# Kernel optimization log

Measured on AMD Instinct MI355X. Metric: run time of the kernel, lower is better.

Reference implementation:

```python
import jax, jax.numpy as jnp
import numpy as np

RX = 1024
RY = 1024
F = 4
HID = 64
N = 2097152


def setup_inputs() -> dict:
    key = jax.random.key(0)
    ks = jax.random.split(key, 8)
    x = jax.random.uniform(ks[0], (N, 3), dtype=jnp.float32)  # (id, u, v) in [0,1)
    emb = jax.random.uniform(ks[1], (RX * RY, F), dtype=jnp.float32) * 2.0 - 1.0
    din = 1 + F  # id feature + interpolated grid feature
    w1 = jax.random.normal(ks[2], (din, HID), dtype=jnp.float32) / np.sqrt(din)
    b1 = jnp.zeros((HID,), dtype=jnp.float32)
    w2 = jax.random.normal(ks[3], (HID, HID), dtype=jnp.float32) / np.sqrt(HID)
    b2 = jnp.zeros((HID,), dtype=jnp.float32)
    w3 = jax.random.normal(ks[4], (HID, 3), dtype=jnp.float32) / np.sqrt(HID)
    b3 = jnp.zeros((3,), dtype=jnp.float32)
    return {"x": x, "emb": emb, "w1": w1, "b1": b1, "w2": w2, "b2": b2, "w3": w3, "b3": b3}


def _grid_features(uv, emb):
    u, v = uv[:, 0], uv[:, 1]
    # vertex ids of bounding cell, faithful to the torch edge handling
    x0 = (u * RX).astype(jnp.int32)
    x0 = jnp.where(x0 == RX, 0, x0)          # wrap exactly-1.0 to 0
    x1 = jnp.where(x0 + 1 == RX, RX - 1, x0 + 1)
    y0 = (v * RY).astype(jnp.int32)
    y1 = jnp.where(y0 + 1 == RY, RY - 1, y0 + 1)
    # weights computed AFTER the x0 wrap, as in the original
    wx = (u * RX - x0.astype(jnp.float32))[:, None]
    wy = (v * RY - y0.astype(jnp.float32))[:, None]
    # four gathers from the flat [RX*RY, F] table (row index = y*RX + x)
    v00 = emb[y0 * RX + x0]
    v10 = emb[y0 * RX + x1]
    v01 = emb[y1 * RX + x0]
    v11 = emb[y1 * RX + x1]
    vup = v00 * (1.0 - wx) + v10 * wx
    vdn = v01 * (1.0 - wx) + v11 * wx
    return vup * (1.0 - wy) + vdn * wy


def reference(x, emb, w1, b1, w2, b2, w3, b3):
    idf = x[:, :1]
    dgf = _grid_features(x[:, 1:3], emb)
    h = jnp.concatenate([idf, dgf], axis=1)   # [N, 5]
    h = jax.nn.relu(h @ w1 + b1)
    h = jax.nn.relu(h @ w2 + b2)
    return jax.nn.sigmoid(h @ w3 + b3)        # [N, 3]
```

## Files before the change

### kernel.cpp

```cpp
#include <hip/hip_runtime.h>
#include <hip/hip_bf16.h>


typedef __attribute__((ext_vector_type(8))) short bf16x8;
typedef __attribute__((ext_vector_type(4))) float f32x4;
typedef __attribute__((ext_vector_type(2))) unsigned int u32x2;
typedef __attribute__((ext_vector_type(4))) unsigned int u32x4;
typedef unsigned long long u64t;

#define HID 64

static __device__ __forceinline__ unsigned short f2bf(float f) {
    __hip_bfloat16 h = __float2bfloat16(f);
    return __builtin_bit_cast(unsigned short, h);
}
static __device__ __forceinline__ unsigned cvt_pk_bf16(float a, float b) {
    unsigned r;
    asm("v_cvt_pk_bf16_f32 %0, %1, %2" : "=v"(r) : "v"(a), "v"(b));
    return r;
}
static __device__ __forceinline__ void lds_fence() {
    asm volatile("s_waitcnt lgkmcnt(0)" ::: "memory");
}
#define MFMA16(a,b,c) __builtin_amdgcn_mfma_f32_16x16x32_bf16((a),(b),(c),0,0,0)

static __device__ __forceinline__ f32x4 unpk2(unsigned lo, unsigned hi) {
    f32x4 r;
    r[0] = __builtin_bit_cast(float, lo << 16);
    r[1] = __builtin_bit_cast(float, lo & 0xFFFF0000u);
    r[2] = __builtin_bit_cast(float, hi << 16);
    r[3] = __builtin_bit_cast(float, hi & 0xFFFF0000u);
    return r;
}
static __device__ __forceinline__ bf16x8 pack_pair(f32x4 lo, f32x4 hi) {
    u32x4 w;
    w[0] = cvt_pk_bf16(fmaxf(lo[0], 0.f), fmaxf(lo[1], 0.f));
    w[1] = cvt_pk_bf16(fmaxf(lo[2], 0.f), fmaxf(lo[3], 0.f));
    w[2] = cvt_pk_bf16(fmaxf(hi[0], 0.f), fmaxf(hi[1], 0.f));
    w[3] = cvt_pk_bf16(fmaxf(hi[2], 0.f), fmaxf(hi[3], 0.f));
    return __builtin_bit_cast(bf16x8, w);
}

struct TFrags {
    bf16x8 a1[4];
    bf16x8 a2[4][2];
    bf16x8 a3[2];
    f32x4  bias2[4];
    f32x4  bias3;
};

static __device__ __forceinline__ void build_tfrags(
    float* Wst, int tid, int cl, int kg,
    const float* __restrict__ w1, const float* __restrict__ b1,
    const float* __restrict__ w2, const float* __restrict__ b2,
    const float* __restrict__ w3, const float* __restrict__ b3, TFrags& F)
{
    {
        const f32x4* w2v = (const f32x4*)w2;
        f32x4* Wv = (f32x4*)Wst;
        #pragma unroll
        for (int i = 0; i < 4; ++i) Wv[tid + 256 * i] = w2v[tid + 256 * i];
        for (int idx = tid; idx < 320; idx += 256) Wst[4096 + idx] = w1[idx];
        if (tid < 64)  Wst[4416 + tid] = b1[tid];
        if (tid < 192) Wst[4480 + tid] = w3[tid];
        if (tid < 64)  Wst[4672 + tid] = b2[tid];
        if (tid < 3)   Wst[4736 + tid] = b3[tid];
    }
    __syncthreads();

    #pragma unroll
    for (int mt = 0; mt < 4; ++mt) {
        bf16x8 f = {};
        if (kg == 0) {
            int hid = mt * 16 + cl;
            #pragma unroll
            for (int j = 0; j < 5; ++j) f[j] = (short)f2bf(Wst[4096 + j * 64 + hid]);
            f[5] = (short)f2bf(Wst[4416 + hid]);
        }
        F.a1[mt] = f;
    }
    #pragma unroll
    for (int ks = 0; ks < 2; ++ks) {
        #pragma unroll
        for (int mt2 = 0; mt2 < 4; ++mt2) {
            bf16x8 f;
            #pragma unroll
            for (int j = 0; j < 8; ++j) {
                int kap = (2 * ks + (j >> 2)) * 16 + kg * 4 + (j & 3);
                f[j] = (short)f2bf(Wst[kap * 64 + mt2 * 16 + cl]);
            }
            F.a2[mt2][ks] = f;
        }
        bf16x8 f3 = {};
        if (cl < 3) {
            #pragma unroll
            for (int j = 0; j < 8; ++j) {
                int kap = (2 * ks + (j >> 2)) * 16 + kg * 4 + (j & 3);
                f3[j] = (short)f2bf(Wst[4480 + kap * 3 + cl]);
            }
        }
        F.a3[ks] = f3;
    }
    #pragma unroll
    for (int mt2 = 0; mt2 < 4; ++mt2) {
        f32x4 b;
        #pragma unroll
        for (int r = 0; r < 4; ++r) b[r] = Wst[4672 + mt2 * 16 + kg * 4 + r];
        F.bias2[mt2] = b;
    }
    {
        f32x4 b = {};
        if (kg == 0) { b[0] = Wst[4736]; b[1] = Wst[4737]; b[2] = Wst[4738]; }
        F.bias3 = b;
    }
    __syncthreads();
}

__global__ __launch_bounds__(256) void conv_dup(const f32x4* __restrict__ emb,
                                                u32x4* __restrict__ tabd) {
    int t = blockIdx.x * 256 + threadIdx.x;
    int y = t >> 10;
    int y1 = (y + 1 > 1023) ? 1023 : y + 1;
    int xx = t & 1023;
    f32x4 a = emb[(y << 10) + xx];
    f32x4 b = emb[(y1 << 10) + xx];
    u32x4 p = {cvt_pk_bf16(a[0], a[1]), cvt_pk_bf16(a[2], a[3]),
               cvt_pk_bf16(b[0], b[1]), cvt_pk_bf16(b[2], b[3])};
    tabd[t] = p;
}

template<int BT>
__global__ __launch_bounds__(256, 3)
void dgn_fused(const float* __restrict__ x, const void* __restrict__ tabv,
               const float* __restrict__ w1, const float* __restrict__ b1,
               const float* __restrict__ w2, const float* __restrict__ b2,
               const float* __restrict__ w3, const float* __restrict__ b3,
               float* __restrict__ out, int n)
{
    __shared__ __align__(16) float Wst[4768];

    const int tid = threadIdx.x, wid = tid >> 6, lane = tid & 63;
    const int cl = lane & 15, kg = lane >> 4;

    TFrags F;
    build_tfrags(Wst, tid, cl, kg, w1, b1, w2, b2, w3, b3, F);

    u32x4* Xf = (u32x4*)Wst + wid * 64;

    const u32x4* __restrict__ tabd = (const u32x4*)tabv;
    const f32x4* __restrict__ tabf = (const f32x4*)tabv;

    const int SP   = gridDim.x * 256;
    const int blk0 = blockIdx.x * 256;
    if (blk0 >= n) return;
    const int iters = (n - blk0 + SP - 1) / SP;
    const int wb0   = blk0 + wid * 64;

    #define LOADX(I, A, B, C) { int pt_ = wb0 + (I) * SP + lane;                \
        int pc_ = pt_ < n ? pt_ : 0; const float* xp_ = x + 3 * pc_;            \
        A = xp_[0]; B = xp_[1]; C = xp_[2]; }

    #define GISSUE(U, V, T0, T1, Fv, WX, WY) {                                  \
        float uf_ = (U) * 1024.f, vf_ = (V) * 1024.f;                           \
        int x0_ = (int)uf_; if (x0_ == 1024) x0_ = 0;                           \
        int x1_ = (x0_ + 1 == 1024) ? 1023 : x0_ + 1;                           \
        int y0_ = (int)vf_;                                                     \
        WX = uf_ - (float)x0_; WY = vf_ - (float)y0_;                           \
        if (y0_ > 1023) y0_ = 1023;                                             \
        int r0_ = y0_ << 10;                                                    \
        if (BT) { T0 = tabd[r0_ + x0_]; T1 = tabd[r0_ + x1_]; }                 \
        else {                                                                  \
            int y1_ = (y0_ + 1 > 1023) ? 1023 : y0_ + 1;                        \
            int r1_ = y1_ << 10;                                                \
            Fv[0] = tabf[r0_ + x0_]; Fv[1] = tabf[r0_ + x1_];                   \
            Fv[2] = tabf[r1_ + x0_]; Fv[3] = tabf[r1_ + x1_]; } }

    u32x4 cT0 = {}, cT1 = {};
    f32x4 cF[4] = {};
    float cwx, cwy, cid;
    float nx0, nx1, nx2;
    {
        float p0, p1, p2;
        LOADX(0, p0, p1, p2);
        GISSUE(p1, p2, cT0, cT1, cF, cwx, cwy);
        cid = p0;
        LOADX(1, nx0, nx1, nx2);
    }

    for (int i = 0; i < iters; ++i) {
        u32x4 tT0 = {}, tT1 = {};
        f32x4 tF[4] = {};
        float twx = 0.f, twy = 0.f, tcid = 0.f;
        const bool more = (i + 1 < iters);
        if (more) {
            GISSUE(nx1, nx2, tT0, tT1, tF, twx, twy);
            tcid = nx0;
            int nix = (i + 2 < iters) ? i + 2 : i + 1;
            LOADX(nix, nx0, nx1, nx2);
        }

        f32x4 A, B, C, D;
        if (BT) {
            A = unpk2(cT0[0], cT0[1]);  C = unpk2(cT0[2], cT0[3]);
            B = unpk2(cT1[0], cT1[1]);  D = unpk2(cT1[2], cT1[3]);
        } else { A = cF[0]; B = cF[1]; C = cF[2]; D = cF[3]; }
        f32x4 up = A + (B - A) * cwx;
        f32x4 dn = C + (D - C) * cwx;
        f32x4 g  = up + (dn - up) * cwy;

        u32x4 inq = {cvt_pk_bf16(cid, g[0]), cvt_pk_bf16(g[1], g[2]),
                     cvt_pk_bf16(g[3], 1.0f), 0u};
        Xf[lane] = inq;
        lds_fence();
        u32x4 bq0 = Xf[0 * 16 + cl];
        u32x4 bq1 = Xf[1 * 16 + cl];
        u32x4 bq2 = Xf[2 * 16 + cl];
        u32x4 bq3 = Xf[3 * 16 + cl];

        const int tb = wb0 + i * SP;
        #pragma unroll
        for (int nt = 0; nt < 4; ++nt) {
            u32x4 bqs = (nt == 0) ? bq0 : (nt == 1) ? bq1 : (nt == 2) ? bq2 : bq3;
            bf16x8 bb = __builtin_bit_cast(bf16x8, bqs);

            f32x4 c1_0 = {}, c1_1 = {}, c1_2 = {}, c1_3 = {};
            c1_0 = MFMA16(F.a1[0], bb, c1_0);
            c1_1 = MFMA16(F.a1[1], bb, c1_1);
            c1_2 = MFMA16(F.a1[2], bb, c1_2);
            c1_3 = MFMA16(F.a1[3], bb, c1_3);

            bf16x8 p0 = pack_pair(c1_0, c1_1);
            bf16x8 p1 = pack_pair(c1_2, c1_3);

            f32x4 c2_0 = F.bias2[0], c2_1 = F.bias2[1],
                  c2_2 = F.bias2[2], c2_3 = F.bias2[3];
            c2_0 = MFMA16(F.a2[0][0], p0, c2_0); c2_0 = MFMA16(F.a2[0][1], p1, c2_0);
            c2_1 = MFMA16(F.a2[1][0], p0, c2_1); c2_1 = MFMA16(F.a2[1][1], p1, c2_1);
            c2_2 = MFMA16(F.a2[2][0], p0, c2_2); c2_2 = MFMA16(F.a2[2][1], p1, c2_2);
            c2_3 = MFMA16(F.a2[3][0], p0, c2_3); c2_3 = MFMA16(F.a2[3][1], p1, c2_3);

            bf16x8 q0 = pack_pair(c2_0, c2_1);
            bf16x8 q1 = pack_pair(c2_2, c2_3);

            f32x4 c3 = F.bias3;
            c3 = MFMA16(F.a3[0], q0, c3);
            c3 = MFMA16(F.a3[1], q1, c3);

            if (kg == 0) {
                int pt = tb + nt * 16 + cl;
                if (pt < n) {
                    #pragma unroll
                    for (int r = 0; r < 3; ++r) {
                        float s = __builtin_amdgcn_rcpf(1.0f + __expf(-c3[r]));
                        out[pt * 3 + r] = s;
                    }
                }
            }
        }

        if (more) {
            cT0 = tT0; cT1 = tT1;
            #pragma unroll
            for (int j = 0; j < 4; ++j) cF[j] = tF[j];
            cwx = twx; cwy = twy; cid = tcid;
        }
    }
    #undef LOADX
    #undef GISSUE
}

extern "C" void kernel_launch(void* const* d_in, const int* in_sizes, int n_in,
                              void* d_out, int out_size, void* d_ws, size_t ws_size,
                              hipStream_t stream) {
    const float* x   = (const float*)d_in[0];
    const float* emb = (const float*)d_in[1];
    const float* w1  = (const float*)d_in[2];
    const float* b1  = (const float*)d_in[3];
    const float* w2  = (const float*)d_in[4];
    const float* b2  = (const float*)d_in[5];
    const float* w3  = (const float*)d_in[6];
    const float* b3  = (const float*)d_in[7];
    float* out = (float*)d_out;

    int n = in_sizes[0] / 3;
    int nblk = (n + 255) / 256;
    if (nblk > 768) nblk = 768;

    const size_t tab_bytes = (size_t)16 * 1024 * 1024;
    if (ws_size >= tab_bytes) {
        conv_dup<<<dim3(4096), dim3(256), 0, stream>>>((const f32x4*)emb, (u32x4*)d_ws);
        dgn_fused<1><<<dim3(nblk), dim3(256), 0, stream>>>(
            x, d_ws, w1, b1, w2, b2, w3, b3, out, n);
    } else {
        dgn_fused<0><<<dim3(nblk), dim3(256), 0, stream>>>(
            x, emb, w1, b1, w2, b2, w3, b3, out, n);
    }
}
```

Before: 66.21 us.

## Deepen gather prefetch pipeline to two iterations ahead and raise grid cap

The software pipeline now issues the embedding-table gathers two iterations ahead instead of one, keeping a second set of in-flight registers so more gather latency is hidden behind MLP compute. The grid cap rises from 768 to 1024 blocks, which changes the per-block iteration count and occupancy spread. The extra in-flight state raises register pressure, which could reduce occupancy. LOADX(2) is issued unconditionally, but it appears to clamp out-of-range points.

```diff
diff --git a/kernel.cpp b/kernel.cpp
--- a/kernel.cpp
+++ b/kernel.cpp
@@ -175,27 +175,33 @@
             Fv[0] = tabf[r0_ + x0_]; Fv[1] = tabf[r0_ + x1_];                   \
             Fv[2] = tabf[r1_ + x0_]; Fv[3] = tabf[r1_ + x1_]; } }
 
-    u32x4 cT0 = {}, cT1 = {};
-    f32x4 cF[4] = {};
-    float cwx, cwy, cid;
+    u32x4 cT0 = {}, cT1 = {}, dT0 = {}, dT1 = {};
+    f32x4 cF[4] = {}, dF[4] = {};
+    float cwx, cwy, cid, dwx, dwy, did;
     float nx0, nx1, nx2;
     {
         float p0, p1, p2;
         LOADX(0, p0, p1, p2);
         GISSUE(p1, p2, cT0, cT1, cF, cwx, cwy);
         cid = p0;
-        LOADX(1, nx0, nx1, nx2);
+        if (iters > 1) {
+            LOADX(1, p0, p1, p2);
+            GISSUE(p1, p2, dT0, dT1, dF, dwx, dwy);
+            did = p0;
+        } else { dwx = dwy = did = 0.f; }
+        LOADX(2, nx0, nx1, nx2);
     }
 
     for (int i = 0; i < iters; ++i) {
-        u32x4 tT0 = {}, tT1 = {};
-        f32x4 tF[4] = {};
-        float twx = 0.f, twy = 0.f, tcid = 0.f;
-        const bool more = (i + 1 < iters);
-        if (more) {
-            GISSUE(nx1, nx2, tT0, tT1, tF, twx, twy);
-            tcid = nx0;
-            int nix = (i + 2 < iters) ? i + 2 : i + 1;
+        u32x4 eT0 = {}, eT1 = {};
+        f32x4 eF[4] = {};
+        float ewx = 0.f, ewy = 0.f, eid = 0.f;
+        const bool more1 = (i + 1 < iters);
+        const bool more2 = (i + 2 < iters);
+        if (more2) {
+            GISSUE(nx1, nx2, eT0, eT1, eF, ewx, ewy);
+            eid = nx0;
+            int nix = (i + 3 < iters) ? i + 3 : i + 2;
             LOADX(nix, nx0, nx1, nx2);
         }
 
@@ -258,11 +264,17 @@
             }
         }
 
-        if (more) {
-            cT0 = tT0; cT1 = tT1;
-            #pragma unroll
-            for (int j = 0; j < 4; ++j) cF[j] = tF[j];
-            cwx = twx; cwy = twy; cid = tcid;
+        if (more1) {
+            cT0 = dT0; cT1 = dT1;
+            #pragma unroll
+            for (int j = 0; j < 4; ++j) cF[j] = dF[j];
+            cwx = dwx; cwy = dwy; cid = did;
+        }
+        if (more2) {
+            dT0 = eT0; dT1 = eT1;
+            #pragma unroll
+            for (int j = 0; j < 4; ++j) dF[j] = eF[j];
+            dwx = ewx; dwy = ewy; did = eid;
         }
     }
     #undef LOADX
@@ -284,7 +296,7 @@
 
     int n = in_sizes[0] / 3;
     int nblk = (n + 255) / 256;
-    if (nblk > 768) nblk = 768;
+    if (nblk > 1024) nblk = 1024;
 
     const size_t tab_bytes = (size_t)16 * 1024 * 1024;
     if (ws_size >= tab_bytes) {
```

Result: slower. 70.64 us (+6.7%).

## Switch MLP and grid table from bf16 to fp16 with packed-half interpolation

Applied to the files above, without the earlier changes.

Converts the duplicated embedding table, weight fragments and MFMA operands from bf16 to fp16, using v_cvt_pkrtz and fp16 MFMA. Bilinear interpolation now runs on packed half2 arithmetic straight from the table words instead of unpacking to fp32, and ReLU is applied after the packed conversion. The aim is fewer ALU instructions per point in the interpolation and activation-pack stages. In exchange it risks fp16 range and precision loss, and round-toward-zero conversion adds bias.

```diff
diff --git a/kernel.cpp b/kernel.cpp
--- a/kernel.cpp
+++ b/kernel.cpp
@@ -2,51 +2,47 @@
 #include <hip/hip_bf16.h>
 
 
-typedef __attribute__((ext_vector_type(8))) short bf16x8;
+typedef _Float16 f16x8 __attribute__((ext_vector_type(8)));
+typedef _Float16 h2v   __attribute__((ext_vector_type(2)));
 typedef __attribute__((ext_vector_type(4))) float f32x4;
-typedef __attribute__((ext_vector_type(2))) unsigned int u32x2;
 typedef __attribute__((ext_vector_type(4))) unsigned int u32x4;
-typedef unsigned long long u64t;
 
 #define HID 64
-
-static __device__ __forceinline__ unsigned short f2bf(float f) {
-    __hip_bfloat16 h = __float2bfloat16(f);
-    return __builtin_bit_cast(unsigned short, h);
-}
-static __device__ __forceinline__ unsigned cvt_pk_bf16(float a, float b) {
-    unsigned r;
-    asm("v_cvt_pk_bf16_f32 %0, %1, %2" : "=v"(r) : "v"(a), "v"(b));
-    return r;
-}
+#define MFMA16H(a,b,c) __builtin_amdgcn_mfma_f32_16x16x32_f16((a),(b),(c),0,0,0)
+
 static __device__ __forceinline__ void lds_fence() {
     asm volatile("s_waitcnt lgkmcnt(0)" ::: "memory");
 }
-#define MFMA16(a,b,c) __builtin_amdgcn_mfma_f32_16x16x32_bf16((a),(b),(c),0,0,0)
-
-static __device__ __forceinline__ f32x4 unpk2(unsigned lo, unsigned hi) {
-    f32x4 r;
-    r[0] = __builtin_bit_cast(float, lo << 16);
-    r[1] = __builtin_bit_cast(float, lo & 0xFFFF0000u);
-    r[2] = __builtin_bit_cast(float, hi << 16);
-    r[3] = __builtin_bit_cast(float, hi & 0xFFFF0000u);
-    return r;
-}
-static __device__ __forceinline__ bf16x8 pack_pair(f32x4 lo, f32x4 hi) {
+static __device__ __forceinline__ unsigned pkrtz_u(float a, float b) {
+    return __builtin_bit_cast(unsigned, __builtin_amdgcn_cvt_pkrtz(a, b));
+}
+static __device__ __forceinline__ h2v u2h(unsigned u) {
+    return __builtin_bit_cast(h2v, u);
+}
+static __device__ __forceinline__ unsigned h2u(h2v h) {
+    return __builtin_bit_cast(unsigned, h);
+}
+static __device__ __forceinline__ unsigned cvtmax(float a, float b) {
+    h2v c = __builtin_bit_cast(h2v, __builtin_amdgcn_cvt_pkrtz(a, b));
+    h2v z = {(_Float16)0.0f, (_Float16)0.0f};
+    c = __builtin_elementwise_max(c, z);
+    return __builtin_bit_cast(unsigned, c);
+}
+static __device__ __forceinline__ f16x8 pack_pair_h(f32x4 lo, f32x4 hi) {
     u32x4 w;
-    w[0] = cvt_pk_bf16(fmaxf(lo[0], 0.f), fmaxf(lo[1], 0.f));
-    w[1] = cvt_pk_bf16(fmaxf(lo[2], 0.f), fmaxf(lo[3], 0.f));
-    w[2] = cvt_pk_bf16(fmaxf(hi[0], 0.f), fmaxf(hi[1], 0.f));
-    w[3] = cvt_pk_bf16(fmaxf(hi[2], 0.f), fmaxf(hi[3], 0.f));
-    return __builtin_bit_cast(bf16x8, w);
+    w[0] = cvtmax(lo[0], lo[1]);
+    w[1] = cvtmax(lo[2], lo[3]);
+    w[2] = cvtmax(hi[0], hi[1]);
+    w[3] = cvtmax(hi[2], hi[3]);
+    return __builtin_bit_cast(f16x8, w);
 }
 
 struct TFrags {
-    bf16x8 a1[4];
-    bf16x8 a2[4][2];
-    bf16x8 a3[2];
-    f32x4  bias2[4];
-    f32x4  bias3;
+    f16x8 a1[4];
+    f16x8 a2[4][2];
+    f16x8 a3[2];
+    f32x4 bias2[4];
+    f32x4 bias3;
 };
 
 static __device__ __forceinline__ void build_tfrags(
@@ -70,12 +66,15 @@
 
     #pragma unroll
     for (int mt = 0; mt < 4; ++mt) {
-        bf16x8 f = {};
+        f16x8 f = {};
         if (kg == 0) {
             int hid = mt * 16 + cl;
-            #pragma unroll
-            for (int j = 0; j < 5; ++j) f[j] = (short)f2bf(Wst[4096 + j * 64 + hid]);
-            f[5] = (short)f2bf(Wst[4416 + hid]);
+            f[0] = (_Float16)Wst[4096 + 0 * 64 + hid];
+            f[1] = (_Float16)Wst[4416 + hid];
+            f[2] = (_Float16)Wst[4096 + 1 * 64 + hid];
+            f[3] = (_Float16)Wst[4096 + 2 * 64 + hid];
+            f[4] = (_Float16)Wst[4096 + 3 * 64 + hid];
+            f[5] = (_Float16)Wst[4096 + 4 * 64 + hid];
         }
         F.a1[mt] = f;
     }
@@ -83,20 +82,20 @@
     for (int ks = 0; ks < 2; ++ks) {
         #pragma unroll
         for (int mt2 = 0; mt2 < 4; ++mt2) {
-            bf16x8 f;
+            f16x8 f;
             #pragma unroll
             for (int j = 0; j < 8; ++j) {
                 int kap = (2 * ks + (j >> 2)) * 16 + kg * 4 + (j & 3);
-                f[j] = (short)f2bf(Wst[kap * 64 + mt2 * 16 + cl]);
+                f[j] = (_Float16)Wst[kap * 64 + mt2 * 16 + cl];
             }
             F.a2[mt2][ks] = f;
         }
-        bf16x8 f3 = {};
+        f16x8 f3 = {};
         if (cl < 3) {
             #pragma unroll
             for (int j = 0; j < 8; ++j) {
                 int kap = (2 * ks + (j >> 2)) * 16 + kg * 4 + (j & 3);
-                f3[j] = (short)f2bf(Wst[4480 + kap * 3 + cl]);
+                f3[j] = (_Float16)Wst[4480 + kap * 3 + cl];
             }
         }
         F.a3[ks] = f3;
@@ -124,8 +123,8 @@
     int xx = t & 1023;
     f32x4 a = emb[(y << 10) + xx];
     f32x4 b = emb[(y1 << 10) + xx];
-    u32x4 p = {cvt_pk_bf16(a[0], a[1]), cvt_pk_bf16(a[2], a[3]),
-               cvt_pk_bf16(b[0], b[1]), cvt_pk_bf16(b[2], b[3])};
+    u32x4 p = {pkrtz_u(a[0], a[1]), pkrtz_u(a[2], a[3]),
+               pkrtz_u(b[0], b[1]), pkrtz_u(b[2], b[3])};
     tabd[t] = p;
 }
 
@@ -199,17 +198,30 @@
             LOADX(nix, nx0, nx1, nx2);
         }
 
-        f32x4 A, B, C, D;
+        u32x4 inq;
         if (BT) {
-            A = unpk2(cT0[0], cT0[1]);  C = unpk2(cT0[2], cT0[3]);
-            B = unpk2(cT1[0], cT1[1]);  D = unpk2(cT1[2], cT1[3]);
-        } else { A = cF[0]; B = cF[1]; C = cF[2]; D = cF[3]; }
-        f32x4 up = A + (B - A) * cwx;
-        f32x4 dn = C + (D - C) * cwx;
-        f32x4 g  = up + (dn - up) * cwy;
-
-        u32x4 inq = {cvt_pk_bf16(cid, g[0]), cvt_pk_bf16(g[1], g[2]),
-                     cvt_pk_bf16(g[3], 1.0f), 0u};
+            _Float16 wxh = (_Float16)cwx, wyh = (_Float16)cwy;
+            h2v wx2 = {wxh, wxh};
+            h2v wy2 = {wyh, wyh};
+            h2v A01 = u2h(cT0[0]), A23 = u2h(cT0[1]);
+            h2v C01 = u2h(cT0[2]), C23 = u2h(cT0[3]);
+            h2v B01 = u2h(cT1[0]), B23 = u2h(cT1[1]);
+            h2v D01 = u2h(cT1[2]), D23 = u2h(cT1[3]);
+            h2v up01 = (B01 - A01) * wx2 + A01;
+            h2v up23 = (B23 - A23) * wx2 + A23;
+            h2v dn01 = (D01 - C01) * wx2 + C01;
+            h2v dn23 = (D23 - C23) * wx2 + C23;
+            h2v g01  = (dn01 - up01) * wy2 + up01;
+            h2v g23  = (dn23 - up23) * wy2 + up23;
+            inq = (u32x4){pkrtz_u(cid, 1.0f), h2u(g01), h2u(g23), 0u};
+        } else {
+            f32x4 A = cF[0], B = cF[1], C = cF[2], D = cF[3];
+            f32x4 up = A + (B - A) * cwx;
+            f32x4 dn = C + (D - C) * cwx;
+            f32x4 g  = up + (dn - up) * cwy;
+            inq = (u32x4){pkrtz_u(cid, 1.0f), pkrtz_u(g[0], g[1]),
+                          pkrtz_u(g[2], g[3]), 0u};
+        }
         Xf[lane] = inq;
         lds_fence();
         u32x4 bq0 = Xf[0 * 16 + cl];
@@ -221,30 +233,30 @@
         #pragma unroll
         for (int nt = 0; nt < 4; ++nt) {
             u32x4 bqs = (nt == 0) ? bq0 : (nt == 1) ? bq1 : (nt == 2) ? bq2 : bq3;
-            bf16x8 bb = __builtin_bit_cast(bf16x8, bqs);
+            f16x8 bb = __builtin_bit_cast(f16x8, bqs);
 
             f32x4 c1_0 = {}, c1_1 = {}, c1_2 = {}, c1_3 = {};
-            c1_0 = MFMA16(F.a1[0], bb, c1_0);
-            c1_1 = MFMA16(F.a1[1], bb, c1_1);
-            c1_2 = MFMA16(F.a1[2], bb, c1_2);
-            c1_3 = MFMA16(F.a1[3], bb, c1_3);
-
-            bf16x8 p0 = pack_pair(c1_0, c1_1);
-            bf16x8 p1 = pack_pair(c1_2, c1_3);
+            c1_0 = MFMA16H(F.a1[0], bb, c1_0);
+            c1_1 = MFMA16H(F.a1[1], bb, c1_1);
+            c1_2 = MFMA16H(F.a1[2], bb, c1_2);
+            c1_3 = MFMA16H(F.a1[3], bb, c1_3);
+
+            f16x8 p0 = pack_pair_h(c1_0, c1_1);
+            f16x8 p1 = pack_pair_h(c1_2, c1_3);
 
             f32x4 c2_0 = F.bias2[0], c2_1 = F.bias2[1],
                   c2_2 = F.bias2[2], c2_3 = F.bias2[3];
-            c2_0 = MFMA16(F.a2[0][0], p0, c2_0); c2_0 = MFMA16(F.a2[0][1], p1, c2_0);
-            c2_1 = MFMA16(F.a2[1][0], p0, c2_1); c2_1 = MFMA16(F.a2[1][1], p1, c2_1);
-            c2_2 = MFMA16(F.a2[2][0], p0, c2_2); c2_2 = MFMA16(F.a2[2][1], p1, c2_2);
-            c2_3 = MFMA16(F.a2[3][0], p0, c2_3); c2_3 = MFMA16(F.a2[3][1], p1, c2_3);
-
-            bf16x8 q0 = pack_pair(c2_0, c2_1);
-            bf16x8 q1 = pack_pair(c2_2, c2_3);
+            c2_0 = MFMA16H(F.a2[0][0], p0, c2_0); c2_0 = MFMA16H(F.a2[0][1], p1, c2_0);
+            c2_1 = MFMA16H(F.a2[1][0], p0, c2_1); c2_1 = MFMA16H(F.a2[1][1], p1, c2_1);
+            c2_2 = MFMA16H(F.a2[2][0], p0, c2_2); c2_2 = MFMA16H(F.a2[2][1], p1, c2_2);
+            c2_3 = MFMA16H(F.a2[3][0], p0, c2_3); c2_3 = MFMA16H(F.a2[3][1], p1, c2_3);
+
+            f16x8 q0 = pack_pair_h(c2_0, c2_1);
+            f16x8 q1 = pack_pair_h(c2_2, c2_3);
 
             f32x4 c3 = F.bias3;
-            c3 = MFMA16(F.a3[0], q0, c3);
-            c3 = MFMA16(F.a3[1], q1, c3);
+            c3 = MFMA16H(F.a3[0], q0, c3);
+            c3 = MFMA16H(F.a3[1], q1, c3);
 
             if (kg == 0) {
                 int pt = tb + nt * 16 + cl;
```

New measurement: 61.44 us. 1.08x faster.
